# Performance work log

Measured on AMD Instinct MI355X. Metric: run time of the kernel, lower is better.

The kernel has to match this reference:

```python
import jax, jax.numpy as jnp
import numpy as np

N_NODES = 100000
N_EDGES = 1600000
WALK_LEN = 16
OUT_DIM = 8
N_PROBES = 32


def setup_inputs() -> dict:
    key = jax.random.key(0)
    k1, k2, k3, k4 = jax.random.split(key, 4)
    edge_index = jax.random.randint(k1, (2, N_EDGES), 0, N_NODES, dtype=jnp.int64 if jax.config.jax_enable_x64 else jnp.int32)
    # Rademacher probes (torch: sign(randn))
    probes = jnp.sign(jax.random.normal(k2, (N_NODES, N_PROBES), dtype=jnp.float32))
    W = jax.random.normal(k3, (OUT_DIM, WALK_LEN), dtype=jnp.float32) * 0.1
    b = jax.random.normal(k4, (OUT_DIM,), dtype=jnp.float32) * 0.1
    return {"edge_index": edge_index, "num_nodes": N_NODES, "probes": probes, "W": W, "b": b}


def reference(edge_index, num_nodes, probes, W, b):
    row, col = edge_index[0], edge_index[1]
    # out-degree of each node, clamped to 1 (as in torch .clamp(min=1))
    deg = jax.ops.segment_sum(jnp.ones(row.shape[0], jnp.float32), row, num_segments=num_nodes)
    deg = jnp.maximum(deg, 1.0)
    rw_values = (1.0 / deg)[row]  # [E] transition weight per edge
    probes_orig = probes

    def step(p, _):
        # gather-scale-scatter: one sparse transition-matrix application
        src = p[row] * rw_values[:, None]                        # [E, P]
        p_new = jax.ops.segment_sum(src, col, num_segments=num_nodes)  # [N, P]
        diag_k = jnp.mean(probes_orig * p_new, axis=1)           # Hutchinson diag estimate [N]
        return p_new, diag_k

    _, diags = jax.lax.scan(step, probes, None, length=WALK_LEN)  # [WALK, N]
    rw_diag = diags.T                                             # [N, WALK]
    return rw_diag @ W.T + b                                      # [N, OUT]
```

## Files before the change

kernel.cpp:

```cpp
#include <hip/hip_runtime.h>

#define N_NODES   100000
#define N_EDGES   1600000
#define WALK_LEN  16
#define OUT_DIM   8
#define N_PROBES  32

#define SCAN_BLK  256
#define NBLK      ((N_NODES + SCAN_BLK - 1) / SCAN_BLK)

#define HB        128
#define SLICE     (N_EDGES / HB)
#define NWORDS    (N_NODES / 4)

#define BURST     16
#define DUMMY     N_NODES
#define CSC_CAP   (N_EDGES + (BURST - 1) * N_NODES)

typedef _Float16 half4 __attribute__((ext_vector_type(4)));
typedef float float2v __attribute__((ext_vector_type(2)));

__device__ __forceinline__ int pad_burst(int x) { return (x + BURST - 1) & ~(BURST - 1); }

__global__ void hist_kernel(const int* __restrict__ arr, unsigned char* __restrict__ partial) {
    __shared__ unsigned int cnt[NWORDS];
    int b = blockIdx.x;
    int t = threadIdx.x;
    for (int i = t; i < NWORDS; i += 1024) cnt[i] = 0;
    __syncthreads();
    const int* a = arr + b * SLICE;
    for (int i = t; i < SLICE; i += 1024) {
        int v = a[i];
        atomicAdd(&cnt[v >> 2], 1u << ((v & 3) * 8));
    }
    __syncthreads();
    unsigned int* dst = (unsigned int*)(partial + (size_t)b * N_NODES);
    for (int i = t; i < NWORDS; i += 1024) dst[i] = cnt[i];
}

__global__ void reduce_out_kernel(const unsigned char* __restrict__ partial,
                                  float* __restrict__ inv_outdeg) {
    int q = blockIdx.x * blockDim.x + threadIdx.x;
    if (q >= NWORDS) return;
    int s0 = 0, s1 = 0, s2 = 0, s3 = 0;
    for (int b = 0; b < HB; b++) {
        unsigned int w = *(const unsigned int*)(partial + (size_t)b * N_NODES + q * 4);
        s0 += w & 0xFF; s1 += (w >> 8) & 0xFF; s2 += (w >> 16) & 0xFF; s3 += (w >> 24) & 0xFF;
    }
    int n = q * 4;
    inv_outdeg[n + 0] = 1.0f / (float)(s0 > 0 ? s0 : 1);
    inv_outdeg[n + 1] = 1.0f / (float)(s1 > 0 ? s1 : 1);
    inv_outdeg[n + 2] = 1.0f / (float)(s2 > 0 ? s2 : 1);
    inv_outdeg[n + 3] = 1.0f / (float)(s3 > 0 ? s3 : 1);
}

__global__ void reduce_scan_col_kernel(unsigned char* __restrict__ partial,
                                       int* __restrict__ indeg) {
    int q = blockIdx.x * blockDim.x + threadIdx.x;
    if (q >= NWORDS) return;
    unsigned int r0 = 0, r1 = 0, r2 = 0, r3 = 0;
    for (int b = 0; b < HB; b++) {
        unsigned int* p = (unsigned int*)(partial + (size_t)b * N_NODES + q * 4);
        unsigned int w = *p;
        *p = (r0 & 0xFF) | ((r1 & 0xFF) << 8) | ((r2 & 0xFF) << 16) | ((r3 & 0xFF) << 24);
        r0 += w & 0xFF; r1 += (w >> 8) & 0xFF; r2 += (w >> 16) & 0xFF; r3 += (w >> 24) & 0xFF;
    }
    int n = q * 4;
    indeg[n + 0] = (int)r0;
    indeg[n + 1] = (int)r1;
    indeg[n + 2] = (int)r2;
    indeg[n + 3] = (int)r3;
}

__global__ void scan1_kernel(const int* __restrict__ indeg, int* __restrict__ bsum) {
    __shared__ int s[SCAN_BLK];
    int i = blockIdx.x * SCAN_BLK + threadIdx.x;
    s[threadIdx.x] = (i < N_NODES) ? pad_burst(indeg[i]) : 0;
    __syncthreads();
    for (int o = SCAN_BLK / 2; o > 0; o >>= 1) {
        if (threadIdx.x < o) s[threadIdx.x] += s[threadIdx.x + o];
        __syncthreads();
    }
    if (threadIdx.x == 0) bsum[blockIdx.x] = s[0];
}

__global__ void scan2_kernel(int* __restrict__ bsum) {
    __shared__ int s[512];
    int t = threadIdx.x;
    s[t] = (t < NBLK) ? bsum[t] : 0;
    __syncthreads();
    for (int o = 1; o < 512; o <<= 1) {
        int v = (t >= o) ? s[t - o] : 0;
        __syncthreads();
        s[t] += v;
        __syncthreads();
    }
    if (t < NBLK) bsum[t] = (t == 0) ? 0 : s[t - 1];
}

__global__ void scan3_kernel(const int* __restrict__ indeg, const int* __restrict__ bsum,
                             int* __restrict__ offs) {
    __shared__ int s[SCAN_BLK];
    int t = threadIdx.x;
    int i = blockIdx.x * SCAN_BLK + t;
    int v = (i < N_NODES) ? pad_burst(indeg[i]) : 0;
    s[t] = v;
    __syncthreads();
    for (int o = 1; o < SCAN_BLK; o <<= 1) {
        int u = (t >= o) ? s[t - o] : 0;
        __syncthreads();
        s[t] += u;
        __syncthreads();
    }
    if (i < N_NODES) offs[i] = bsum[blockIdx.x] + s[t] - v;
}

__global__ void fill_dummy_kernel(int* __restrict__ csc_row) {
    int i = blockIdx.x * blockDim.x + threadIdx.x;
    if (i >= CSC_CAP / 4) return;
    reinterpret_cast<int4*>(csc_row)[i] = make_int4(DUMMY, DUMMY, DUMMY, DUMMY);
}

__global__ void place_kernel(const int* __restrict__ row, const int* __restrict__ col,
                             const int* __restrict__ offs,
                             const unsigned char* __restrict__ pbase,
                             int* __restrict__ csc_row) {
    __shared__ unsigned int cnt[NWORDS];
    int b = blockIdx.x;
    int t = threadIdx.x;
    const unsigned int* src = (const unsigned int*)(pbase + (size_t)b * N_NODES);
    for (int i = t; i < NWORDS; i += 1024) cnt[i] = src[i];
    __syncthreads();
    for (int i = t; i < SLICE; i += 1024) {
        int e = b * SLICE + i;
        int c = col[e];
        int sh = (c & 3) * 8;
        unsigned int old = atomicAdd(&cnt[c >> 2], 1u << sh);
        int pos = (int)((old >> sh) & 0xFF);
        csc_row[offs[c] + pos] = row[e];
    }
}

__global__ void pack_kernel(const float* __restrict__ probes, unsigned int* __restrict__ pbits) {
    int n = blockIdx.x * blockDim.x + threadIdx.x;
    if (n >= N_NODES) return;
    unsigned int bits = 0;
    const float* p = probes + (size_t)n * N_PROBES;
#pragma unroll
    for (int i = 0; i < N_PROBES; i++) bits |= (p[i] < 0.0f) ? (1u << i) : 0u;
    pbits[n] = bits;
}

__global__ void s0_kernel(const float* __restrict__ probes, const float* __restrict__ inv_outdeg,
                          _Float16* __restrict__ s0) {
    int gid = blockIdx.x * blockDim.x + threadIdx.x;
    int n = gid >> 3;
    int j = (gid & 7) << 2;
    float iv = inv_outdeg[n];
    const float4 p = *reinterpret_cast<const float4*>(probes + (size_t)n * N_PROBES + j);
    half4 h;
    h[0] = (_Float16)(p.x * iv); h[1] = (_Float16)(p.y * iv);
    h[2] = (_Float16)(p.z * iv); h[3] = (_Float16)(p.w * iv);
    *reinterpret_cast<half4*>(s0 + (size_t)n * N_PROBES + j) = h;
}

__global__ void zero_dummy_kernel(_Float16* __restrict__ s0h,
                                  unsigned int* __restrict__ a8, unsigned int* __restrict__ b8) {
    int t = threadIdx.x;
    if (t < 16)      reinterpret_cast<unsigned int*>(s0h + (size_t)DUMMY * N_PROBES)[t] = 0u;
    else if (t < 24) a8[(size_t)DUMMY * 8 + (t - 16)] = 0u;
    else if (t < 32) b8[(size_t)DUMMY * 8 + (t - 24)] = 0u;
}

template <bool IN8>
__global__ void gather_kernel(const int* __restrict__ offs, const int* __restrict__ indeg,
                              const int* __restrict__ csc_row,
                              const void* __restrict__ s_cur,
                              const unsigned int* __restrict__ pbits,
                              const float* __restrict__ inv_outdeg,
                              unsigned int* __restrict__ s_new, float* __restrict__ diag_row) {
    int gid = blockIdx.x * blockDim.x + threadIdx.x;
    int n = gid >> 3;
    int lane = gid & 7;
    int start = offs[n];
    int pcnt  = pad_burst(indeg[n]);
    float inv = inv_outdeg[n];
    float4 acc = make_float4(0.f, 0.f, 0.f, 0.f);

    const _Float16*     h_base = (const _Float16*)s_cur;
    const unsigned int* q_base = (const unsigned int*)s_cur;

    int r[BURST];
    if (pcnt > 0) {
#pragma unroll
        for (int u = 0; u < BURST; u++)
            r[u] = __builtin_nontemporal_load(&csc_row[start + u]);
    }
    for (int q = 0; q < pcnt; q += BURST) {
        half4        vh[BURST];
        unsigned int vq[BURST];
#pragma unroll
        for (int u = 0; u < BURST; u++) {
            if (IN8) vq[u] = q_base[(size_t)r[u] * 8 + lane];
            else     vh[u] = *reinterpret_cast<const half4*>(h_base + (size_t)r[u] * N_PROBES + lane * 4);
        }
        int r2[BURST];
        if (q + BURST < pcnt) {
#pragma unroll
            for (int u = 0; u < BURST; u++)
                r2[u] = __builtin_nontemporal_load(&csc_row[start + q + BURST + u]);
        }
#pragma unroll
        for (int u = 0; u < BURST; u++) {
            if (IN8) {
                float2v lo = __builtin_amdgcn_cvt_pk_f32_fp8((int)vq[u], false);
                float2v hi = __builtin_amdgcn_cvt_pk_f32_fp8((int)vq[u], true);
                acc.x += lo[0]; acc.y += lo[1]; acc.z += hi[0]; acc.w += hi[1];
            } else {
                acc.x += (float)vh[u][0]; acc.y += (float)vh[u][1];
                acc.z += (float)vh[u][2]; acc.w += (float)vh[u][3];
            }
        }
#pragma unroll
        for (int u = 0; u < BURST; u++) r[u] = r2[u];
    }

    int pk = 0;
    pk = __builtin_amdgcn_cvt_pk_fp8_f32(acc.x * inv, acc.y * inv, pk, false);
    pk = __builtin_amdgcn_cvt_pk_fp8_f32(acc.z * inv, acc.w * inv, pk, true);
    s_new[(size_t)n * 8 + lane] = (unsigned int)pk;

    unsigned int bits = pbits[n] >> (lane << 2);
    float d0 = (bits & 1u) ? -acc.x : acc.x;
    float d1 = (bits & 2u) ? -acc.y : acc.y;
    float d2 = (bits & 4u) ? -acc.z : acc.z;
    float d3 = (bits & 8u) ? -acc.w : acc.w;
    float dot = d0 + d1 + d2 + d3;
    dot += __shfl_xor(dot, 4, 8);
    dot += __shfl_xor(dot, 2, 8);
    dot += __shfl_xor(dot, 1, 8);
    if (lane == 0) diag_row[n] = dot * (1.0f / (float)N_PROBES);
}

__global__ void out_kernel(const float* __restrict__ diags, const float* __restrict__ W,
                           const float* __restrict__ b, float* __restrict__ out) {
    int n = blockIdx.x * blockDim.x + threadIdx.x;
    if (n >= N_NODES) return;
    float d[WALK_LEN];
#pragma unroll
    for (int k = 0; k < WALK_LEN; k++) d[k] = diags[(size_t)k * N_NODES + n];
    float o[OUT_DIM];
#pragma unroll
    for (int j = 0; j < OUT_DIM; j++) {
        float acc = b[j];
#pragma unroll
        for (int k = 0; k < WALK_LEN; k++) acc += d[k] * W[j * WALK_LEN + k];
        o[j] = acc;
    }
    float4* outp = reinterpret_cast<float4*>(out + (size_t)n * OUT_DIM);
    outp[0] = make_float4(o[0], o[1], o[2], o[3]);
    outp[1] = make_float4(o[4], o[5], o[6], o[7]);
}

extern "C" void kernel_launch(void* const* d_in, const int* in_sizes, int n_in,
                              void* d_out, int out_size, void* d_ws, size_t ws_size,
                              hipStream_t stream) {
    const int*   edge_index = (const int*)d_in[0];
    const int*   row    = edge_index;
    const int*   col    = edge_index + N_EDGES;
    const float* probes = (const float*)d_in[2];
    const float* W      = (const float*)d_in[3];
    const float* b      = (const float*)d_in[4];
    float*       out    = (float*)d_out;

    char* ws = (char*)d_ws;
    size_t off = 0;
    auto carve = [&](size_t bytes) -> void* {
        void* p = ws + off;
        off += (bytes + 255) & ~(size_t)255;
        return p;
    };
    int*           indeg   = (int*)          carve((size_t)N_NODES * 4);
    int*           offs    = (int*)          carve((size_t)N_NODES * 4);
    float*         inv_od  = (float*)        carve((size_t)N_NODES * 4);
    int*           bsum    = (int*)          carve((size_t)NBLK * 4);
    unsigned char* partial = (unsigned char*)carve((size_t)HB * N_NODES);
    int*           csc_row = (int*)          carve((size_t)CSC_CAP * 4);
    _Float16*      s0h     = (_Float16*)     carve((size_t)(N_NODES + 1) * N_PROBES * 2);
    unsigned int*  bufA8   = (unsigned int*) carve((size_t)(N_NODES + 1) * 32);
    unsigned int*  bufB8   = (unsigned int*) carve((size_t)(N_NODES + 1) * 32);
    float*         diags   = (float*)        carve((size_t)WALK_LEN * N_NODES * 4);
    unsigned int*  pbits   = (unsigned int*) carve((size_t)N_NODES * 4);

    const int B = 256;
    hist_kernel<<<HB, 1024, 0, stream>>>(row, partial);
    reduce_out_kernel<<<(NWORDS + B - 1) / B, B, 0, stream>>>(partial, inv_od);
    hist_kernel<<<HB, 1024, 0, stream>>>(col, partial);
    reduce_scan_col_kernel<<<(NWORDS + B - 1) / B, B, 0, stream>>>(partial, indeg);
    scan1_kernel<<<NBLK, SCAN_BLK, 0, stream>>>(indeg, bsum);
    scan2_kernel<<<1, 512, 0, stream>>>(bsum);
    scan3_kernel<<<NBLK, SCAN_BLK, 0, stream>>>(indeg, bsum, offs);
    fill_dummy_kernel<<<(CSC_CAP / 4 + B - 1) / B, B, 0, stream>>>(csc_row);
    place_kernel<<<HB, 1024, 0, stream>>>(row, col, offs, partial, csc_row);

    pack_kernel<<<(N_NODES + B - 1) / B, B, 0, stream>>>(probes, pbits);
    s0_kernel<<<(N_NODES * 8 + B - 1) / B, B, 0, stream>>>(probes, inv_od, s0h);
    zero_dummy_kernel<<<1, 64, 0, stream>>>(s0h, bufA8, bufB8);

    const int GRID = (N_NODES * 8 + B - 1) / B;
    gather_kernel<false><<<GRID, B, 0, stream>>>(offs, indeg, csc_row, (const void*)s0h,
                                                 pbits, inv_od, bufA8, diags);
    const unsigned int* cur = bufA8;
    for (int k = 1; k < WALK_LEN; k++) {
        unsigned int* nxt = (k & 1) ? bufB8 : bufA8;
        gather_kernel<true><<<GRID, B, 0, stream>>>(offs, indeg, csc_row, (const void*)cur,
                                                    pbits, inv_od, nxt, diags + (size_t)k * N_NODES);
        cur = nxt;
    }

    out_kernel<<<(N_NODES + B - 1) / B, B, 0, stream>>>(diags, W, b, out);
}
```

Baseline: 472.7 us.

## Fuse histogram, reduce and probe-prep kernels; add launch bounds to gather

```diff
diff --git a/kernel.cpp b/kernel.cpp
--- a/kernel.cpp
+++ b/kernel.cpp
@@ -12,6 +12,7 @@
 #define HB        128
 #define SLICE     (N_EDGES / HB)
 #define NWORDS    (N_NODES / 4)
+#define RB        ((NWORDS + 255) / 256)
 
 #define BURST     16
 #define DUMMY     N_NODES
@@ -22,9 +23,14 @@
 
 __device__ __forceinline__ int pad_burst(int x) { return (x + BURST - 1) & ~(BURST - 1); }
 
-__global__ void hist_kernel(const int* __restrict__ arr, unsigned char* __restrict__ partial) {
+__global__ void hist2_kernel(const int* __restrict__ row, const int* __restrict__ col,
+                             unsigned char* __restrict__ partialR,
+                             unsigned char* __restrict__ partialC) {
     __shared__ unsigned int cnt[NWORDS];
-    int b = blockIdx.x;
+    int blk = blockIdx.x;
+    const int* arr = (blk < HB) ? row : col;
+    unsigned char* partial = (blk < HB) ? partialR : partialC;
+    int b = (blk < HB) ? blk : blk - HB;
     int t = threadIdx.x;
     for (int i = t; i < NWORDS; i += 1024) cnt[i] = 0;
     __syncthreads();
@@ -38,38 +44,40 @@
     for (int i = t; i < NWORDS; i += 1024) dst[i] = cnt[i];
 }
 
-__global__ void reduce_out_kernel(const unsigned char* __restrict__ partial,
-                                  float* __restrict__ inv_outdeg) {
-    int q = blockIdx.x * blockDim.x + threadIdx.x;
-    if (q >= NWORDS) return;
-    int s0 = 0, s1 = 0, s2 = 0, s3 = 0;
-    for (int b = 0; b < HB; b++) {
-        unsigned int w = *(const unsigned int*)(partial + (size_t)b * N_NODES + q * 4);
-        s0 += w & 0xFF; s1 += (w >> 8) & 0xFF; s2 += (w >> 16) & 0xFF; s3 += (w >> 24) & 0xFF;
-    }
-    int n = q * 4;
-    inv_outdeg[n + 0] = 1.0f / (float)(s0 > 0 ? s0 : 1);
-    inv_outdeg[n + 1] = 1.0f / (float)(s1 > 0 ? s1 : 1);
-    inv_outdeg[n + 2] = 1.0f / (float)(s2 > 0 ? s2 : 1);
-    inv_outdeg[n + 3] = 1.0f / (float)(s3 > 0 ? s3 : 1);
-}
-
-__global__ void reduce_scan_col_kernel(unsigned char* __restrict__ partial,
-                                       int* __restrict__ indeg) {
-    int q = blockIdx.x * blockDim.x + threadIdx.x;
-    if (q >= NWORDS) return;
-    unsigned int r0 = 0, r1 = 0, r2 = 0, r3 = 0;
-    for (int b = 0; b < HB; b++) {
-        unsigned int* p = (unsigned int*)(partial + (size_t)b * N_NODES + q * 4);
-        unsigned int w = *p;
-        *p = (r0 & 0xFF) | ((r1 & 0xFF) << 8) | ((r2 & 0xFF) << 16) | ((r3 & 0xFF) << 24);
-        r0 += w & 0xFF; r1 += (w >> 8) & 0xFF; r2 += (w >> 16) & 0xFF; r3 += (w >> 24) & 0xFF;
-    }
-    int n = q * 4;
-    indeg[n + 0] = (int)r0;
-    indeg[n + 1] = (int)r1;
-    indeg[n + 2] = (int)r2;
-    indeg[n + 3] = (int)r3;
+__global__ void reduce2_kernel(const unsigned char* __restrict__ partialR,
+                               float* __restrict__ inv_outdeg,
+                               unsigned char* __restrict__ partialC,
+                               int* __restrict__ indeg) {
+    int blk = blockIdx.x;
+    if (blk < RB) {
+        int q = blk * 256 + threadIdx.x;
+        if (q >= NWORDS) return;
+        int s0 = 0, s1 = 0, s2 = 0, s3 = 0;
+        for (int b = 0; b < HB; b++) {
+            unsigned int w = *(const unsigned int*)(partialR + (size_t)b * N_NODES + q * 4);
+            s0 += w & 0xFF; s1 += (w >> 8) & 0xFF; s2 += (w >> 16) & 0xFF; s3 += (w >> 24) & 0xFF;
+        }
+        int n = q * 4;
+        inv_outdeg[n + 0] = 1.0f / (float)(s0 > 0 ? s0 : 1);
+        inv_outdeg[n + 1] = 1.0f / (float)(s1 > 0 ? s1 : 1);
+        inv_outdeg[n + 2] = 1.0f / (float)(s2 > 0 ? s2 : 1);
+        inv_outdeg[n + 3] = 1.0f / (float)(s3 > 0 ? s3 : 1);
+    } else {
+        int q = (blk - RB) * 256 + threadIdx.x;
+        if (q >= NWORDS) return;
+        unsigned int r0 = 0, r1 = 0, r2 = 0, r3 = 0;
+        for (int b = 0; b < HB; b++) {
+            unsigned int* p = (unsigned int*)(partialC + (size_t)b * N_NODES + q * 4);
+            unsigned int w = *p;
+            *p = (r0 & 0xFF) | ((r1 & 0xFF) << 8) | ((r2 & 0xFF) << 16) | ((r3 & 0xFF) << 24);
+            r0 += w & 0xFF; r1 += (w >> 8) & 0xFF; r2 += (w >> 16) & 0xFF; r3 += (w >> 24) & 0xFF;
+        }
+        int n = q * 4;
+        indeg[n + 0] = (int)r0;
+        indeg[n + 1] = (int)r1;
+        indeg[n + 2] = (int)r2;
+        indeg[n + 3] = (int)r3;
+    }
 }
 
 __global__ void scan1_kernel(const int* __restrict__ indeg, int* __restrict__ bsum) {
@@ -141,19 +149,13 @@
     }
 }
 
-__global__ void pack_kernel(const float* __restrict__ probes, unsigned int* __restrict__ pbits) {
-    int n = blockIdx.x * blockDim.x + threadIdx.x;
-    if (n >= N_NODES) return;
-    unsigned int bits = 0;
-    const float* p = probes + (size_t)n * N_PROBES;
-#pragma unroll
-    for (int i = 0; i < N_PROBES; i++) bits |= (p[i] < 0.0f) ? (1u << i) : 0u;
-    pbits[n] = bits;
-}
-
-__global__ void s0_kernel(const float* __restrict__ probes, const float* __restrict__ inv_outdeg,
-                          _Float16* __restrict__ s0) {
+__global__ void s0pack_kernel(const float* __restrict__ probes, const float* __restrict__ inv_outdeg,
+                              _Float16* __restrict__ s0h, unsigned int* __restrict__ pbits,
+                              unsigned int* __restrict__ a8, unsigned int* __restrict__ b8) {
     int gid = blockIdx.x * blockDim.x + threadIdx.x;
+    if (gid < 16)      reinterpret_cast<unsigned int*>(s0h + (size_t)DUMMY * N_PROBES)[gid] = 0u;
+    else if (gid < 24) a8[(size_t)DUMMY * 8 + (gid - 16)] = 0u;
+    else if (gid < 32) b8[(size_t)DUMMY * 8 + (gid - 24)] = 0u;
     int n = gid >> 3;
     int j = (gid & 7) << 2;
     float iv = inv_outdeg[n];
@@ -161,24 +163,24 @@
     half4 h;
     h[0] = (_Float16)(p.x * iv); h[1] = (_Float16)(p.y * iv);
     h[2] = (_Float16)(p.z * iv); h[3] = (_Float16)(p.w * iv);
-    *reinterpret_cast<half4*>(s0 + (size_t)n * N_PROBES + j) = h;
-}
-
-__global__ void zero_dummy_kernel(_Float16* __restrict__ s0h,
-                                  unsigned int* __restrict__ a8, unsigned int* __restrict__ b8) {
-    int t = threadIdx.x;
-    if (t < 16)      reinterpret_cast<unsigned int*>(s0h + (size_t)DUMMY * N_PROBES)[t] = 0u;
-    else if (t < 24) a8[(size_t)DUMMY * 8 + (t - 16)] = 0u;
-    else if (t < 32) b8[(size_t)DUMMY * 8 + (t - 24)] = 0u;
+    *reinterpret_cast<half4*>(s0h + (size_t)n * N_PROBES + j) = h;
+    unsigned int b4 = (p.x < 0.f ? 1u : 0u) | (p.y < 0.f ? 2u : 0u) |
+                      (p.z < 0.f ? 4u : 0u) | (p.w < 0.f ? 8u : 0u);
+    unsigned int bits = b4 << j;
+    bits |= __shfl_xor(bits, 1, 8);
+    bits |= __shfl_xor(bits, 2, 8);
+    bits |= __shfl_xor(bits, 4, 8);
+    if ((gid & 7) == 0) pbits[n] = bits;
 }
 
 template <bool IN8>
-__global__ void gather_kernel(const int* __restrict__ offs, const int* __restrict__ indeg,
-                              const int* __restrict__ csc_row,
-                              const void* __restrict__ s_cur,
-                              const unsigned int* __restrict__ pbits,
-                              const float* __restrict__ inv_outdeg,
-                              unsigned int* __restrict__ s_new, float* __restrict__ diag_row) {
+__global__ __launch_bounds__(256, 7)
+void gather_kernel(const int* __restrict__ offs, const int* __restrict__ indeg,
+                   const int* __restrict__ csc_row,
+                   const void* __restrict__ s_cur,
+                   const unsigned int* __restrict__ pbits,
+                   const float* __restrict__ inv_outdeg,
+                   unsigned int* __restrict__ s_new, float* __restrict__ diag_row) {
     int gid = blockIdx.x * blockDim.x + threadIdx.x;
     int n = gid >> 3;
     int lane = gid & 7;
@@ -201,8 +203,8 @@
         unsigned int vq[BURST];
 #pragma unroll
         for (int u = 0; u < BURST; u++) {
-            if (IN8) vq[u] = q_base[(size_t)r[u] * 8 + lane];
-            else     vh[u] = *reinterpret_cast<const half4*>(h_base + (size_t)r[u] * N_PROBES + lane * 4);
+            if (IN8) vq[u] = q_base[r[u] * 8 + lane];
+            else     vh[u] = *reinterpret_cast<const half4*>(h_base + r[u] * N_PROBES + lane * 4);
         }
         int r2[BURST];
         if (q + BURST < pcnt) {
@@ -228,7 +230,7 @@
     int pk = 0;
     pk = __builtin_amdgcn_cvt_pk_fp8_f32(acc.x * inv, acc.y * inv, pk, false);
     pk = __builtin_amdgcn_cvt_pk_fp8_f32(acc.z * inv, acc.w * inv, pk, true);
-    s_new[(size_t)n * 8 + lane] = (unsigned int)pk;
+    s_new[n * 8 + lane] = (unsigned int)pk;
 
     unsigned int bits = pbits[n] >> (lane << 2);
     float d0 = (bits & 1u) ? -acc.x : acc.x;
@@ -280,32 +282,30 @@
         off += (bytes + 255) & ~(size_t)255;
         return p;
     };
-    int*           indeg   = (int*)          carve((size_t)N_NODES * 4);
-    int*           offs    = (int*)          carve((size_t)N_NODES * 4);
-    float*         inv_od  = (float*)        carve((size_t)N_NODES * 4);
-    int*           bsum    = (int*)          carve((size_t)NBLK * 4);
-    unsigned char* partial = (unsigned char*)carve((size_t)HB * N_NODES);
-    int*           csc_row = (int*)          carve((size_t)CSC_CAP * 4);
-    _Float16*      s0h     = (_Float16*)     carve((size_t)(N_NODES + 1) * N_PROBES * 2);
-    unsigned int*  bufA8   = (unsigned int*) carve((size_t)(N_NODES + 1) * 32);
-    unsigned int*  bufB8   = (unsigned int*) carve((size_t)(N_NODES + 1) * 32);
-    float*         diags   = (float*)        carve((size_t)WALK_LEN * N_NODES * 4);
-    unsigned int*  pbits   = (unsigned int*) carve((size_t)N_NODES * 4);
+    int*           indeg    = (int*)          carve((size_t)N_NODES * 4);
+    int*           offs     = (int*)          carve((size_t)N_NODES * 4);
+    float*         inv_od   = (float*)        carve((size_t)N_NODES * 4);
+    int*           bsum     = (int*)          carve((size_t)NBLK * 4);
+    unsigned char* partialR = (unsigned char*)carve((size_t)HB * N_NODES);
+    unsigned char* partialC = (unsigned char*)carve((size_t)HB * N_NODES);
+    int*           csc_row  = (int*)          carve((size_t)CSC_CAP * 4);
+    _Float16*      s0h      = (_Float16*)     carve((size_t)(N_NODES + 1) * N_PROBES * 2);
+    unsigned int*  bufA8    = (unsigned int*) carve((size_t)(N_NODES + 1) * 32);
+    unsigned int*  bufB8    = (unsigned int*) carve((size_t)(N_NODES + 1) * 32);
+    float*         diags    = (float*)        carve((size_t)WALK_LEN * N_NODES * 4);
+    unsigned int*  pbits    = (unsigned int*) carve((size_t)N_NODES * 4);
 
     const int B = 256;
-    hist_kernel<<<HB, 1024, 0, stream>>>(row, partial);
-    reduce_out_kernel<<<(NWORDS + B - 1) / B, B, 0, stream>>>(partial, inv_od);
-    hist_kernel<<<HB, 1024, 0, stream>>>(col, partial);
-    reduce_scan_col_kernel<<<(NWORDS + B - 1) / B, B, 0, stream>>>(partial, indeg);
+    hist2_kernel<<<2 * HB, 1024, 0, stream>>>(row, col, partialR, partialC);
+    reduce2_kernel<<<2 * RB, B, 0, stream>>>(partialR, inv_od, partialC, indeg);
     scan1_kernel<<<NBLK, SCAN_BLK, 0, stream>>>(indeg, bsum);
     scan2_kernel<<<1, 512, 0, stream>>>(bsum);
     scan3_kernel<<<NBLK, SCAN_BLK, 0, stream>>>(indeg, bsum, offs);
     fill_dummy_kernel<<<(CSC_CAP / 4 + B - 1) / B, B, 0, stream>>>(csc_row);
-    place_kernel<<<HB, 1024, 0, stream>>>(row, col, offs, partial, csc_row);
-
-    pack_kernel<<<(N_NODES + B - 1) / B, B, 0, stream>>>(probes, pbits);
-    s0_kernel<<<(N_NODES * 8 + B - 1) / B, B, 0, stream>>>(probes, inv_od, s0h);
-    zero_dummy_kernel<<<1, 64, 0, stream>>>(s0h, bufA8, bufB8);
+    place_kernel<<<HB, 1024, 0, stream>>>(row, col, offs, partialC, csc_row);
+
+    s0pack_kernel<<<(N_NODES * 8 + B - 1) / B, B, 0, stream>>>(probes, inv_od, s0h,
+                                                               pbits, bufA8, bufB8);
 
     const int GRID = (N_NODES * 8 + B - 1) / B;
     gather_kernel<false><<<GRID, B, 0, stream>>>(offs, indeg, csc_row, (const void*)s0h,
```

Result: slower. 936.4 us (+98.1%).
